# Kernel tuning notes

Measured on AMD Instinct MI355X. Metric: run time of the kernel, lower is better.

The kernel has to match this reference:

```python
import jax, jax.numpy as jnp
import numpy as np

B, S, H, E, V, T = 64, 256, 1024, 512, 10000, 64
D = H // 2  # per-direction LSTM hidden


def setup_inputs() -> dict:
    key = jax.random.key(0)
    ks = jax.random.split(key, 16)
    s = jnp.float32(0.02)
    emb = jax.random.normal(ks[4], (V, E), jnp.float32) * s
    emb = emb.at[0].set(0.0)  # padding_idx=0
    return {
        "encoder_outputs": jax.random.normal(ks[0], (B, S, H), jnp.float32),
        "enc_h0": jax.random.normal(ks[1], (2, B, D), jnp.float32),
        "enc_c0": jax.random.normal(ks[2], (2, B, D), jnp.float32),
        "target": jax.random.randint(ks[3], (B, T), 1, V),
        "mask": jnp.zeros((B, S), jnp.bool_),
        "sos_idx": 1,
        "emb": emb,
        "Wa": jax.random.normal(ks[5], (H, H), jnp.float32) * s,
        "Ua": jax.random.normal(ks[6], (H, H), jnp.float32) * s,
        "Va": jax.random.normal(ks[7], (H,), jnp.float32) * s,
        "out_W": jax.random.normal(ks[8], (V, H), jnp.float32) * s,
        "out_b": jnp.zeros((V,), jnp.float32),
        "Wih_f": jax.random.normal(ks[9], (4 * D, E + H), jnp.float32) * s,
        "Whh_f": jax.random.normal(ks[10], (4 * D, D), jnp.float32) * s,
        "bih_f": jnp.zeros((4 * D,), jnp.float32),
        "bhh_f": jnp.zeros((4 * D,), jnp.float32),
        "Wih_b": jax.random.normal(ks[11], (4 * D, E + H), jnp.float32) * s,
        "Whh_b": jax.random.normal(ks[12], (4 * D, D), jnp.float32) * s,
        "bih_b": jnp.zeros((4 * D,), jnp.float32),
        "bhh_b": jnp.zeros((4 * D,), jnp.float32),
    }


def _lstm_cell(x, h, c, Wih, Whh, bih, bhh):
    g = x @ Wih.T + h @ Whh.T + bih + bhh
    i, f, gg, o = jnp.split(g, 4, axis=-1)  # torch gate order i,f,g,o
    c2 = jax.nn.sigmoid(f) * c + jax.nn.sigmoid(i) * jnp.tanh(gg)
    h2 = jax.nn.sigmoid(o) * jnp.tanh(c2)
    return h2, c2


def reference(encoder_outputs, enc_h0, enc_c0, target, mask, sos_idx, emb, Wa, Ua, Va,
              out_W, out_b, Wih_f, Whh_f, bih_f, bhh_f, Wih_b, Whh_b, bih_b, bhh_b):
    # Cache Ua(keys) once (original recomputes it each step; math identical).
    Uk = jnp.einsum('bsh,kh->bsk', encoder_outputs, Ua)  # [B,S,H]
    b = encoder_outputs.shape[0]
    tokens = jnp.concatenate(
        [jnp.full((b, 1), sos_idx, target.dtype), target[:, :-1]], axis=1)  # [B,T]
    xs = tokens.T  # [T,B]

    def step(carry, tok):
        h, c = carry  # each [2,B,D]
        query = jnp.swapaxes(h, 0, 1).reshape(b, -1)  # [B,H] (fwd||bwd)
        sc = jnp.einsum('bsh,h->bs', jnp.tanh((query @ Wa.T)[:, None, :] + Uk), Va)
        sc = jnp.where(mask, -jnp.inf, sc)
        w = jax.nn.softmax(sc, axis=-1)  # [B,S]
        ctx = jnp.einsum('bs,bsh->bh', w, encoder_outputs)  # [B,H]
        x = jnp.concatenate([emb[tok], ctx], axis=-1)  # [B,E+H]
        hf, cf = _lstm_cell(x, h[0], c[0], Wih_f, Whh_f, bih_f, bhh_f)
        hb, cb = _lstm_cell(x, h[1], c[1], Wih_b, Whh_b, bih_b, bhh_b)
        out = jnp.concatenate([hf, hb], axis=-1)  # [B,H]
        logits = out @ out_W.T + out_b  # [B,V]
        return (jnp.stack([hf, hb]), jnp.stack([cf, cb])), (logits, w)

    (h, c), (logits, attns) = jax.lax.scan(step, (enc_h0, enc_c0), xs)
    decoder_outputs = jnp.swapaxes(logits, 0, 1)  # [B,T,V]
    attentions = jnp.swapaxes(attns, 0, 1)        # [B,T,S]
    return decoder_outputs, h, c, attentions
```

## Files before the change

kernel.cpp:

```cpp
#include <hip/hip_runtime.h>

#define NB 64
#define NS 256
#define NH 1024
#define NE 512
#define NV 10000
#define NT 64
#define ND 512
#define NEH 1536

typedef __attribute__((ext_vector_type(8))) short bf16x8;
typedef __attribute__((ext_vector_type(4))) float f32x4;

__device__ __forceinline__ short F2B(float f) {
  unsigned u = __float_as_uint(f);
  return (short)((u + 0x7fffu + ((u >> 16) & 1u)) >> 16);
}
__device__ __forceinline__ float B2F(short s) {
  return __uint_as_float(((unsigned)(unsigned short)s) << 16);
}
__device__ __forceinline__ float ftanh(float x) {
  float e = __expf(2.f * x);
  return 1.f - 2.f * __builtin_amdgcn_rcpf(e + 1.f);
}

#define GLD16(src, dst)                                                        \
  __builtin_amdgcn_global_load_lds(                                            \
      (const __attribute__((address_space(1))) void*)(src),                    \
      (__attribute__((address_space(3))) void*)(dst), 16, 0, 0)

__device__ __forceinline__ void mm64_f32a(
    const float* __restrict__ Af, int lda, const short* __restrict__ Wg,
    int ldw, int K, short* Ch, size_t ldc, char* smem)
{
  const int tid = threadIdx.x;
  const int lane = tid & 63, w = tid >> 6;
  const int qm = (w >> 1) << 5, qn = (w & 1) << 5;
  const int kg = lane >> 4, rl = lane & 15;
  f32x4 acc[2][2] = {};
  const int nIt = K >> 6;

  auto stage = [&](int k0, int buf) {
    char* As = smem + (buf << 14);
    char* Bs = As + 8192;
#pragma unroll
    for (int p = 0; p < 2; ++p) {
      int j = tid + (p << 8);
      int row = j >> 3;
      int c = (j & 7) ^ (row & 7);
      const float* src = Af + (size_t)row * lda + k0 + (c << 3);
      float4 v0 = ((const float4*)src)[0];
      float4 v1 = ((const float4*)src)[1];
      bf16x8 pk;
      pk[0] = F2B(v0.x); pk[1] = F2B(v0.y); pk[2] = F2B(v0.z); pk[3] = F2B(v0.w);
      pk[4] = F2B(v1.x); pk[5] = F2B(v1.y); pk[6] = F2B(v1.z); pk[7] = F2B(v1.w);
      *((bf16x8*)As + j) = pk;
    }
#pragma unroll
    for (int p = 0; p < 2; ++p) {
      int j = (w << 7) + (p << 6) + lane;
      int row = j >> 3;
      int c = (j & 7) ^ (row & 7);
      GLD16(Wg + (size_t)row * ldw + k0 + (c << 3), Bs + (w << 11) + (p << 10));
    }
  };

  stage(0, 0);
  for (int it = 0; it < nIt; ++it) {
    __syncthreads();
    if (it + 1 < nIt) stage((it + 1) << 6, (it + 1) & 1);
    const short* As = (const short*)(smem + ((it & 1) << 14));
    const short* Bs = As + 4096;
#pragma unroll
    for (int kk = 0; kk < 2; ++kk) {
      bf16x8 af[2], bfr[2];
#pragma unroll
      for (int mt = 0; mt < 2; ++mt) {
        int r2 = qm + (mt << 4) + rl;
        int c = (kk << 2) + kg;
        af[mt] = *((const bf16x8*)As + ((r2 << 3) | (c ^ (r2 & 7))));
      }
#pragma unroll
      for (int nt = 0; nt < 2; ++nt) {
        int r2 = qn + (nt << 4) + rl;
        int c = (kk << 2) + kg;
        bfr[nt] = *((const bf16x8*)Bs + ((r2 << 3) | (c ^ (r2 & 7))));
      }
#pragma unroll
      for (int mt = 0; mt < 2; ++mt)
#pragma unroll
        for (int nt = 0; nt < 2; ++nt)
          acc[mt][nt] = __builtin_amdgcn_mfma_f32_16x16x32_bf16(
              af[mt], bfr[nt], acc[mt][nt], 0, 0, 0);
    }
  }
#pragma unroll
  for (int mt = 0; mt < 2; ++mt)
#pragma unroll
    for (int nt = 0; nt < 2; ++nt) {
      int cn = qn + (nt << 4) + rl;
#pragma unroll
      for (int r = 0; r < 4; ++r) {
        int rowm = qm + (mt << 4) + (kg << 2) + r;
        Ch[(size_t)rowm * ldc + cn] = F2B(acc[mt][nt][r]);
      }
    }
}

__global__ __launch_bounds__(256) void uk_mm_f32(const float* __restrict__ enc,
                                                 const short* __restrict__ Ua_h,
                                                 short* __restrict__ Uk_h) {
  __shared__ char smem[32768];
  mm64_f32a(enc + (size_t)blockIdx.y * 64 * NH, NH,
            Ua_h + (size_t)blockIdx.x * 64 * NH, NH, NH,
            Uk_h + (size_t)blockIdx.y * 64 * NH + blockIdx.x * 64, NH, smem);
}

template <int MODE>
__global__ __launch_bounds__(256) void mm128(
    const short* __restrict__ A, const short* __restrict__ Bw, int nvmax,
    const float* __restrict__ bias, float* __restrict__ Cf,
    short* __restrict__ Ch)
{
  __shared__ char smem[32768];
  const int tid = threadIdx.x, lane = tid & 63, w = tid >> 6;
  const int m0 = blockIdx.y << 7;
  const int n0 = blockIdx.x << 7;
  const int qm = (w >> 1) << 6, qn = (w & 1) << 6;
  const int kg = lane >> 4, rl = lane & 15;
  f32x4 acc[4][4] = {};
  for (int k0 = 0; k0 < NH; k0 += 64) {
#pragma unroll
    for (int p = 0; p < 4; ++p) {
      int j = (((w << 2) + p) << 6) + lane;
      int row = j >> 3;
      int c = (j & 7) ^ (row & 7);
      GLD16(A + (size_t)(m0 + row) * NH + k0 + (c << 3),
            smem + (((w << 2) + p) << 10));
      int vr = n0 + row; if (vr > nvmax - 1) vr = nvmax - 1;
      GLD16(Bw + (size_t)vr * NH + k0 + (c << 3),
            smem + 16384 + (((w << 2) + p) << 10));
    }
    __syncthreads();
    const short* As = (const short*)smem;
    const short* Bs = (const short*)(smem + 16384);
#pragma unroll
    for (int kk = 0; kk < 2; ++kk) {
      bf16x8 af[4], bfr[4];
#pragma unroll
      for (int mt = 0; mt < 4; ++mt) {
        int r2 = qm + (mt << 4) + rl;
        int c = (kk << 2) + kg;
        af[mt] = *((const bf16x8*)As + ((r2 << 3) | (c ^ (r2 & 7))));
      }
#pragma unroll
      for (int nt = 0; nt < 4; ++nt) {
        int r2 = qn + (nt << 4) + rl;
        int c = (kk << 2) + kg;
        bfr[nt] = *((const bf16x8*)Bs + ((r2 << 3) | (c ^ (r2 & 7))));
      }
#pragma unroll
      for (int mt = 0; mt < 4; ++mt)
#pragma unroll
        for (int nt = 0; nt < 4; ++nt)
          acc[mt][nt] = __builtin_amdgcn_mfma_f32_16x16x32_bf16(
              af[mt], bfr[nt], acc[mt][nt], 0, 0, 0);
    }
    __syncthreads();
  }
#pragma unroll
  for (int nt = 0; nt < 4; ++nt) {
    int colv = n0 + qn + (nt << 4) + rl;
    if (colv < nvmax) {
#pragma unroll
      for (int mt = 0; mt < 4; ++mt)
#pragma unroll
        for (int r = 0; r < 4; ++r) {
          int m = m0 + qm + (mt << 4) + (kg << 2) + r;
          if (MODE == 0) {
            int b = m & 63, t = m >> 6;
            Cf[(size_t)((b << 6) + t) * NV + colv] = acc[mt][nt][r] + bias[colv];
          } else {
            Ch[(size_t)m * NH + colv] = F2B(acc[mt][nt][r]);
          }
        }
    }
  }
}

__global__ __launch_bounds__(256) void gates_v2(
    const short* __restrict__ Xt, const short* __restrict__ hcur,
    const short* __restrict__ Wcomb, const float* __restrict__ bperm,
    const float* __restrict__ cq_old, float* __restrict__ hq_f,
    float* __restrict__ cq_new, short* __restrict__ hnext)
{
  __shared__ char smem[61440];
  const int tid = threadIdx.x, lane = tid & 63, w = tid >> 6;
  const int kg = lane >> 4, rl = lane & 15;
  const int dir = blockIdx.x >> 7, gi = blockIdx.x & 127;
  const int hoff = dir << 9;
  const short* Wbase = Wcomb + (((size_t)(dir << 11) + (gi << 4)) << 11);

  auto stage = [&](int it, int buf) {
    char* dst = smem + buf * 20480;
#pragma unroll
    for (int g = 0; g < 4; ++g) {
      int row = (g << 4) + (w << 2) + kg;
      int c = rl ^ (row & 15);
      int k = (it << 7) + (c << 3);
      const short* src = (k < NEH) ? (Xt + (size_t)row * NEH + k)
                                   : (hcur + (size_t)row * NH + hoff + (k - NEH));
      GLD16(src, dst + (g << 12) + (w << 10));
    }
    {
      int rowB = (w << 2) + kg;
      int cB = rl ^ rowB;
      int kB = (it << 7) + (cB << 3);
      GLD16(Wbase + (size_t)rowB * 2048 + kB, dst + 16384 + (w << 10));
    }
  };

  stage(0, 0); stage(1, 1); stage(2, 2);
  f32x4 acc = {};
  int buf = 0;
  for (int it = 0; it < 16; ++it) {
    if (it < 14)      asm volatile("s_waitcnt vmcnt(10)" ::: "memory");
    else if (it == 14) asm volatile("s_waitcnt vmcnt(5)" ::: "memory");
    else               asm volatile("s_waitcnt vmcnt(0)" ::: "memory");
    __builtin_amdgcn_s_barrier();
    __builtin_amdgcn_sched_barrier(0);
    const short* As = (const short*)(smem + buf * 20480);
    const short* Bs = (const short*)(smem + buf * 20480 + 16384);
    const int rowA = (w << 4) + rl;
#pragma unroll
    for (int kk = 0; kk < 4; ++kk) {
      int chunk = (kk << 2) | kg;
      bf16x8 af = *((const bf16x8*)As + ((rowA << 4) | (chunk ^ (rowA & 15))));
      bf16x8 bf = *((const bf16x8*)Bs + ((rl << 4) | (chunk ^ rl)));
      acc = __builtin_amdgcn_mfma_f32_16x16x32_bf16(af, bf, acc, 0, 0, 0);
    }
    __builtin_amdgcn_sched_barrier(0);
    __builtin_amdgcn_s_barrier();
    if (it + 3 < 16) stage(it + 3, buf);
    buf = (buf == 2) ? 0 : buf + 1;
  }
  float* gacc = (float*)smem;
#pragma unroll
  for (int r = 0; r < 4; ++r)
    gacc[((w << 4) + (kg << 2) + r) * 17 + rl] = acc[r];
  __syncthreads();
  {
    const int b = tid >> 2, j2 = tid & 3;
    const float* bp = bperm + (dir << 11) + (gi << 4) + (j2 << 2);
    const float* gr = gacc + b * 17 + (j2 << 2);
    float gi_ = gr[0] + bp[0];
    float gf_ = gr[1] + bp[1];
    float gg_ = gr[2] + bp[2];
    float go_ = gr[3] + bp[3];
    const int d = ((gi >> 2) << 4) + (((gi << 2) + j2) & 15);
    const int idx = (b << 10) + hoff + d;
    float c0v = cq_old[idx];
    float si = 1.f / (1.f + __expf(-gi_));
    float sf = 1.f / (1.f + __expf(-gf_));
    float so = 1.f / (1.f + __expf(-go_));
    float tg = ftanh(gg_);
    float c2 = sf * c0v + si * tg;
    float h2 = so * ftanh(c2);
    hq_f[idx] = h2;
    cq_new[idx] = c2;
    hnext[idx] = F2B(h2);
  }
}

__global__ __launch_bounds__(256) void q_mm2(const short* __restrict__ hcur,
                                             const short* __restrict__ Wa_h,
                                             float* __restrict__ q)
{
  __shared__ char smem[61440];
  const int tid = threadIdx.x, lane = tid & 63, w = tid >> 6;
  const int kg = lane >> 4, rl = lane & 15;
  const int n0 = blockIdx.x << 4;
  const short* Wbase = Wa_h + (size_t)n0 * NH;

  auto stage = [&](int it, int buf) {
    char* dst = smem + buf * 20480;
#pragma unroll
    for (int g = 0; g < 4; ++g) {
      int row = (g << 4) + (w << 2) + kg;
      int c = rl ^ (row & 15);
      int k = (it << 7) + (c << 3);
      GLD16(hcur + (size_t)row * NH + k, dst + (g << 12) + (w << 10));
    }
    {
      int rowB = (w << 2) + kg;
      int cB = rl ^ rowB;
      int kB = (it << 7) + (cB << 3);
      GLD16(Wbase + (size_t)rowB * NH + kB, dst + 16384 + (w << 10));
    }
  };

  stage(0, 0); stage(1, 1); stage(2, 2);
  f32x4 acc = {};
  int buf = 0;
  for (int it = 0; it < 8; ++it) {
    if (it < 6)       asm volatile("s_waitcnt vmcnt(10)" ::: "memory");
    else if (it == 6) asm volatile("s_waitcnt vmcnt(5)" ::: "memory");
    else              asm volatile("s_waitcnt vmcnt(0)" ::: "memory");
    __builtin_amdgcn_s_barrier();
    __builtin_amdgcn_sched_barrier(0);
    const short* As = (const short*)(smem + buf * 20480);
    const short* Bs = (const short*)(smem + buf * 20480 + 16384);
    const int rowA = (w << 4) + rl;
#pragma unroll
    for (int kk = 0; kk < 4; ++kk) {
      int chunk = (kk << 2) | kg;
      bf16x8 af = *((const bf16x8*)As + ((rowA << 4) | (chunk ^ (rowA & 15))));
      bf16x8 bf = *((const bf16x8*)Bs + ((rl << 4) | (chunk ^ rl)));
      acc = __builtin_amdgcn_mfma_f32_16x16x32_bf16(af, bf, acc, 0, 0, 0);
    }
    __builtin_amdgcn_sched_barrier(0);
    __builtin_amdgcn_s_barrier();
    if (it + 3 < 8) stage(it + 3, buf);
    buf = (buf == 2) ? 0 : buf + 1;
  }
#pragma unroll
  for (int r = 0; r < 4; ++r)
    q[(size_t)((w << 4) + (kg << 2) + r) * NH + n0 + rl] = acc[r];
}

__global__ __launch_bounds__(256) void f2b_k(const float* __restrict__ in,
                                             short* __restrict__ out, int n4) {
  int i = blockIdx.x * 256 + threadIdx.x;
  const int stride = gridDim.x * 256;
  for (; i < n4; i += stride) {
    float4 v = ((const float4*)in)[i];
    short4 o;
    o.x = F2B(v.x); o.y = F2B(v.y); o.z = F2B(v.z); o.w = F2B(v.w);
    ((short4*)out)[i] = o;
  }
}

__global__ __launch_bounds__(256) void perm_w(
    const float* __restrict__ Wih_f, const float* __restrict__ Whh_f,
    const float* __restrict__ Wih_b, const float* __restrict__ Whh_b,
    const float* __restrict__ bih_f, const float* __restrict__ bhh_f,
    const float* __restrict__ bih_b, const float* __restrict__ bhh_b,
    short* __restrict__ Wcomb, float* __restrict__ bias_perm)
{
  int i = blockIdx.x * 256 + threadIdx.x;
  int k4 = i & 511;
  int np = (i >> 9) & 2047;
  int dir = i >> 20;
  int gate = np & 3, dlo = (np >> 2) & 15, dblk = np >> 6;
  int d = (dblk << 4) + dlo;
  int r = (gate << 9) + d;
  int k = k4 << 2;
  const float* Wih = dir ? Wih_b : Wih_f;
  const float* Whh = dir ? Whh_b : Whh_f;
  float4 v = (k < NEH) ? *(const float4*)(Wih + (size_t)r * NEH + k)
                       : *(const float4*)(Whh + (size_t)r * ND + (k - NEH));
  short4 o;
  o.x = F2B(v.x); o.y = F2B(v.y); o.z = F2B(v.z); o.w = F2B(v.w);
  *(short4*)(Wcomb + ((size_t)((dir << 11) + np) << 11) + k) = o;
  if (k4 == 0) {
    const float* bi = dir ? bih_b : bih_f;
    const float* bh = dir ? bhh_b : bhh_f;
    bias_perm[(dir << 11) + np] = bi[r] + bh[r];
  }
}

__global__ __launch_bounds__(256) void emb_fill(
    const float* __restrict__ emb, const int* __restrict__ target,
    const int* __restrict__ sos, short* __restrict__ Xbuf)
{
  int idx = blockIdx.x * 256 + threadIdx.x;
  int t = idx >> 13;
  int r = idx & 8191;
  int b = r >> 7, e4 = r & 127;
  int tok = (t == 0) ? sos[0] : target[b * NT + t - 1];
  float4 v = *(const float4*)(emb + (size_t)tok * NE + (e4 << 2));
  short4 o;
  o.x = F2B(v.x); o.y = F2B(v.y); o.z = F2B(v.z); o.w = F2B(v.w);
  *(short4*)(Xbuf + (size_t)(t * NB + b) * NEH + (e4 << 2)) = o;
}

__global__ __launch_bounds__(256) void init_state(
    const float* __restrict__ h0, const float* __restrict__ c0,
    float* __restrict__ hq, float* __restrict__ cq, short* __restrict__ H0) {
  int idx = blockIdx.x * 256 + threadIdx.x;
  int b = idx >> 10, dir = (idx >> 9) & 1, d = idx & 511;
  int src = dir * NB * ND + (b << 9) + d;
  float h = h0[src];
  hq[idx] = h;
  cq[idx] = c0[src];
  H0[idx] = F2B(h);
}

__global__ __launch_bounds__(256) void final_state(
    const float* __restrict__ hq, const float* __restrict__ cq,
    float* __restrict__ out_h, float* __restrict__ out_c) {
  int idx = blockIdx.x * 256 + threadIdx.x;
  int dir = idx >> 15, r = idx & 32767, b = r >> 9, d = r & 511;
  int src = b * NH + dir * ND + d;
  out_h[idx] = hq[src];
  out_c[idx] = cq[src];
}

__global__ __launch_bounds__(256) void attn_score(
    const float* __restrict__ q, const short* __restrict__ Uk,
    const float* __restrict__ Va, const unsigned char* __restrict__ mask,
    float* __restrict__ sc) {
  __shared__ float qs[NH];
  const int b = blockIdx.x >> 6;
  {
    int t4 = threadIdx.x << 2;
    *(float4*)(qs + t4) = *(const float4*)(q + (size_t)b * NH + t4);
  }
  __syncthreads();
  const int lane = threadIdx.x & 63, wid = threadIdx.x >> 6;
  const int bs = (blockIdx.x << 2) + wid;
  const short* ukp = Uk + (size_t)bs * NH;
  float acc = 0.f;
#pragma unroll
  for (int i = 0; i < 2; ++i) {
    int h = (i << 9) + (lane << 3);
    bf16x8 uv = *(const bf16x8*)(ukp + h);
    float4 q0 = *(const float4*)(qs + h);
    float4 q1 = *(const float4*)(qs + h + 4);
    float4 v0 = *(const float4*)(Va + h);
    float4 v1 = *(const float4*)(Va + h + 4);
    acc += v0.x * ftanh(q0.x + B2F(uv[0]));
    acc += v0.y * ftanh(q0.y + B2F(uv[1]));
    acc += v0.z * ftanh(q0.z + B2F(uv[2]));
    acc += v0.w * ftanh(q0.w + B2F(uv[3]));
    acc += v1.x * ftanh(q1.x + B2F(uv[4]));
    acc += v1.y * ftanh(q1.y + B2F(uv[5]));
    acc += v1.z * ftanh(q1.z + B2F(uv[6]));
    acc += v1.w * ftanh(q1.w + B2F(uv[7]));
  }
#pragma unroll
  for (int o = 32; o; o >>= 1) acc += __shfl_down(acc, o);
  if (lane == 0) sc[bs] = mask[bs] ? -__builtin_inff() : acc;
}

__global__ __launch_bounds__(256) void ctx_soft(
    const float* __restrict__ sc, const float* __restrict__ enc_f,
    const short* __restrict__ enc_h, int use_h,
    short* __restrict__ Xt, float* __restrict__ attn_out, int t) {
  const int tid = threadIdx.x;
  const int b = blockIdx.x >> 2, qh = blockIdx.x & 3;
  __shared__ float red[4];
  __shared__ float ws[NS];
  __shared__ float4 red4[4][64];
  float v = sc[b * NS + tid];
  float m = v;
#pragma unroll
  for (int o = 32; o; o >>= 1) m = fmaxf(m, __shfl_down(m, o));
  if ((tid & 63) == 0) red[tid >> 6] = m;
  __syncthreads();
  m = fmaxf(fmaxf(red[0], red[1]), fmaxf(red[2], red[3]));
  float e = __expf(v - m);
  float su = e;
#pragma unroll
  for (int o = 32; o; o >>= 1) su += __shfl_down(su, o);
  __syncthreads();
  if ((tid & 63) == 0) red[tid >> 6] = su;
  __syncthreads();
  su = red[0] + red[1] + red[2] + red[3];
  float wgt = e / su;
  ws[tid] = wgt;
  if (qh == 0) attn_out[((size_t)b * NT + t) * NS + tid] = wgt;
  __syncthreads();
  const int w = tid >> 6, l = tid & 63;
  const int h = (qh << 8) + (l << 2);
  const int s0 = w << 6;
  float4 a = make_float4(0.f, 0.f, 0.f, 0.f);
  if (use_h) {
    const short* ep = enc_h + ((size_t)b * NS + s0) * NH + h;
    for (int s = 0; s < 64; ++s) {
      short4 vv = *(const short4*)(ep + (size_t)s * NH);
      float wv = ws[s0 + s];
      a.x += wv * B2F(vv.x); a.y += wv * B2F(vv.y);
      a.z += wv * B2F(vv.z); a.w += wv * B2F(vv.w);
    }
  } else {
    const float* ep = enc_f + ((size_t)b * NS + s0) * NH + h;
    for (int s = 0; s < 64; ++s) {
      float4 vv = *(const float4*)(ep + (size_t)s * NH);
      float wv = ws[s0 + s];
      a.x += wv * vv.x; a.y += wv * vv.y; a.z += wv * vv.z; a.w += wv * vv.w;
    }
  }
  red4[w][l] = a;
  __syncthreads();
  if (tid < 64) {
    float4 r0 = red4[0][tid], r1 = red4[1][tid], r2 = red4[2][tid],
           r3 = red4[3][tid];
    short4 o;
    o.x = F2B(r0.x + r1.x + r2.x + r3.x);
    o.y = F2B(r0.y + r1.y + r2.y + r3.y);
    o.z = F2B(r0.z + r1.z + r2.z + r3.z);
    o.w = F2B(r0.w + r1.w + r2.w + r3.w);
    *(short4*)(Xt + (size_t)b * NEH + NE + (qh << 8) + (tid << 2)) = o;
  }
}

extern "C" void kernel_launch(void* const* d_in, const int* in_sizes, int n_in,
                              void* d_out, int out_size, void* d_ws, size_t ws_size,
                              hipStream_t stream)
{
  const float* enc    = (const float*)d_in[0];
  const float* h0     = (const float*)d_in[1];
  const float* c0     = (const float*)d_in[2];
  const int*   target = (const int*)d_in[3];
  const unsigned char* mask = (const unsigned char*)d_in[4];
  const int*   sos    = (const int*)d_in[5];
  const float* emb    = (const float*)d_in[6];
  const float* Wa     = (const float*)d_in[7];
  const float* Ua     = (const float*)d_in[8];
  const float* Va     = (const float*)d_in[9];
  const float* out_W  = (const float*)d_in[10];
  const float* out_b  = (const float*)d_in[11];
  const float* Wih_f  = (const float*)d_in[12];
  const float* Whh_f  = (const float*)d_in[13];
  const float* bih_f  = (const float*)d_in[14];
  const float* bhh_f  = (const float*)d_in[15];
  const float* Wih_b  = (const float*)d_in[16];
  const float* Whh_b  = (const float*)d_in[17];
  const float* bih_b  = (const float*)d_in[18];
  const float* bhh_b  = (const float*)d_in[19];

  float* out_dec  = (float*)d_out;
  float* out_h    = out_dec + (size_t)NB * NT * NV;
  float* out_c    = out_h + 2 * NB * ND;
  float* out_attn = out_c + 2 * NB * ND;

  char* base = (char*)d_ws;
  size_t off = 0;
  auto alloc = [&](size_t bytes) -> char* {
    char* p = base + off;
    off += (bytes + 255) & ~(size_t)255;
    return p;
  };
  short* Uk_h  = (short*)alloc((size_t)NB * NS * NH * 2);
  short* ow_h  = (short*)alloc((size_t)NV * NH * 2);
  short* Ua_h  = (short*)alloc((size_t)NH * NH * 2);
  short* Wa_h  = (short*)alloc((size_t)NH * NH * 2);
  short* Wcomb = (short*)alloc((size_t)2 * 2048 * 2048 * 2);
  float* bperm = (float*)alloc((size_t)2 * 2048 * 4);
  float* q     = (float*)alloc((size_t)NB * NH * 4);
  float* sc    = (float*)alloc((size_t)NB * NS * 4);
  short* Xbuf  = (short*)alloc((size_t)NT * NB * NEH * 2);
  float* hq    = (float*)alloc((size_t)NB * NH * 4);
  float* cq    = (float*)alloc((size_t)2 * NB * NH * 4);
  short* Hbuf  = (short*)alloc((size_t)(NT + 1) * NB * NH * 2);
  short* enc_h = nullptr;
  int use_h = 0;
  if (off + (size_t)NB * NS * NH * 2 <= ws_size) {
    enc_h = (short*)alloc((size_t)NB * NS * NH * 2);
    use_h = 1;
  }
  if (off > ws_size) return;

  f2b_k<<<dim3(2048), dim3(256), 0, stream>>>(out_W, ow_h, NV * NH / 4);
  f2b_k<<<dim3(1024), dim3(256), 0, stream>>>(Ua, Ua_h, NH * NH / 4);
  f2b_k<<<dim3(1024), dim3(256), 0, stream>>>(Wa, Wa_h, NH * NH / 4);
  perm_w<<<dim3(8192), dim3(256), 0, stream>>>(Wih_f, Whh_f, Wih_b, Whh_b,
                                               bih_f, bhh_f, bih_b, bhh_b,
                                               Wcomb, bperm);
  emb_fill<<<dim3(2048), dim3(256), 0, stream>>>(emb, target, sos, Xbuf);
  init_state<<<dim3(256), dim3(256), 0, stream>>>(h0, c0, hq, cq, Hbuf);
  if (use_h) {
    f2b_k<<<dim3(2048), dim3(256), 0, stream>>>(enc, enc_h, NB * NS * NH / 4);
    mm128<1><<<dim3(8, 128), dim3(256), 0, stream>>>(enc_h, Ua_h, NH, nullptr,
                                                     nullptr, Uk_h);
  } else {
    uk_mm_f32<<<dim3(16, 256), dim3(256), 0, stream>>>(enc, Ua_h, Uk_h);
  }

  for (int t = 0; t < NT; ++t) {
    const short* hcur = Hbuf + (size_t)t * NB * NH;
    short* hnext = Hbuf + (size_t)(t + 1) * NB * NH;
    float* cq_cur = cq + (t & 1) * (NB * NH);
    float* cq_nxt = cq + ((t & 1) ^ 1) * (NB * NH);
    short* Xt = Xbuf + (size_t)t * NB * NEH;

    q_mm2<<<dim3(64), dim3(256), 0, stream>>>(hcur, Wa_h, q);
    attn_score<<<dim3(4096), dim3(256), 0, stream>>>(q, Uk_h, Va, mask, sc);
    ctx_soft<<<dim3(256), dim3(256), 0, stream>>>(sc, enc, enc_h, use_h,
                                                  Xt, out_attn, t);
    gates_v2<<<dim3(256), dim3(256), 0, stream>>>(Xt, hcur, Wcomb, bperm,
                                                  cq_cur, hq, cq_nxt, hnext);
  }

  mm128<0><<<dim3(79, 32), dim3(256), 0, stream>>>(Hbuf + NB * NH, ow_h, NV,
                                                   out_b, out_dec, nullptr);
  final_state<<<dim3(256), dim3(256), 0, stream>>>(hq, cq, out_h, out_c);
}
```

Baseline: 2.095 ms.

## Fuse attention score, softmax and context into one per-batch kernel

Replaces the separate score kernel and softmax/context kernel with a single kernel using one 1024-thread block per batch row. Scores stay in shared memory, removing one launch per step and the global score round-trip. The grid shrinks to 64 blocks, so each block must stream its full Uk and encoder slices. This risks underusing the GPU's compute units and memory bandwidth.

```diff
diff --git a/kernel.cpp b/kernel.cpp
--- a/kernel.cpp
+++ b/kernel.cpp
@@ -328,6 +328,82 @@
     q[(size_t)((w << 4) + (kg << 2) + r) * NH + n0 + rl] = acc[r];
 }
 
+__global__ __launch_bounds__(1024) void attn_fused(
+    const float* __restrict__ q, const short* __restrict__ Uk,
+    const float* __restrict__ Va, const unsigned char* __restrict__ mask,
+    const short* __restrict__ enc_h, const float* __restrict__ enc_f,
+    int use_h, short* __restrict__ Xt, float* __restrict__ attn_out, int t)
+{
+  __shared__ float scs[NS];
+  __shared__ float ws[NS];
+  const int tid = threadIdx.x;
+  const int lane = tid & 63, w = tid >> 6;
+  const int b = blockIdx.x;
+
+  float qv[16], vv[16];
+  {
+    const float* qp = q + (size_t)b * NH + (lane << 4);
+    const float* vp = Va + (lane << 4);
+#pragma unroll
+    for (int j4 = 0; j4 < 4; ++j4) {
+      float4 a = *(const float4*)(qp + (j4 << 2));
+      float4 c = *(const float4*)(vp + (j4 << 2));
+      qv[(j4 << 2) + 0] = a.x; qv[(j4 << 2) + 1] = a.y;
+      qv[(j4 << 2) + 2] = a.z; qv[(j4 << 2) + 3] = a.w;
+      vv[(j4 << 2) + 0] = c.x; vv[(j4 << 2) + 1] = c.y;
+      vv[(j4 << 2) + 2] = c.z; vv[(j4 << 2) + 3] = c.w;
+    }
+  }
+
+#pragma unroll 1
+  for (int i = 0; i < 16; ++i) {
+    const int s = (w << 4) + i;
+    const short* up = Uk + ((size_t)b * NS + s) * NH + (lane << 4);
+    bf16x8 u0 = ((const bf16x8*)up)[0];
+    bf16x8 u1 = ((const bf16x8*)up)[1];
+    float a = 0.f;
+#pragma unroll
+    for (int j = 0; j < 8; ++j) a += vv[j] * ftanh(qv[j] + B2F(u0[j]));
+#pragma unroll
+    for (int j = 0; j < 8; ++j) a += vv[8 + j] * ftanh(qv[8 + j] + B2F(u1[j]));
+#pragma unroll
+    for (int o = 32; o; o >>= 1) a += __shfl_down(a, o);
+    if (lane == 0) scs[s] = mask[b * NS + s] ? -__builtin_inff() : a;
+  }
+  __syncthreads();
+
+  if (w == 0) {
+    float v0 = scs[lane], v1 = scs[lane + 64], v2 = scs[lane + 128],
+          v3 = scs[lane + 192];
+    float m = fmaxf(fmaxf(v0, v1), fmaxf(v2, v3));
+#pragma unroll
+    for (int o = 32; o; o >>= 1) m = fmaxf(m, __shfl_xor(m, o));
+    float e0 = __expf(v0 - m), e1 = __expf(v1 - m);
+    float e2 = __expf(v2 - m), e3 = __expf(v3 - m);
+    float su = e0 + e1 + e2 + e3;
+#pragma unroll
+    for (int o = 32; o; o >>= 1) su += __shfl_xor(su, o);
+    float inv = 1.f / su;
+    e0 *= inv; e1 *= inv; e2 *= inv; e3 *= inv;
+    ws[lane] = e0; ws[lane + 64] = e1; ws[lane + 128] = e2; ws[lane + 192] = e3;
+    float* ap = attn_out + ((size_t)b * NT + t) * NS;
+    ap[lane] = e0; ap[lane + 64] = e1; ap[lane + 128] = e2; ap[lane + 192] = e3;
+  }
+  __syncthreads();
+
+  float acc = 0.f;
+  if (use_h) {
+    const short* ep = enc_h + (size_t)b * NS * NH + tid;
+#pragma unroll 4
+    for (int s = 0; s < NS; ++s) acc += ws[s] * B2F(ep[(size_t)s * NH]);
+  } else {
+    const float* ep = enc_f + (size_t)b * NS * NH + tid;
+#pragma unroll 4
+    for (int s = 0; s < NS; ++s) acc += ws[s] * ep[(size_t)s * NH];
+  }
+  Xt[(size_t)b * NEH + NE + tid] = F2B(acc);
+}
+
 __global__ __launch_bounds__(256) void f2b_k(const float* __restrict__ in,
                                              short* __restrict__ out, int n4) {
   int i = blockIdx.x * 256 + threadIdx.x;
@@ -404,105 +480,6 @@
   int src = b * NH + dir * ND + d;
   out_h[idx] = hq[src];
   out_c[idx] = cq[src];
-}
-
-__global__ __launch_bounds__(256) void attn_score(
-    const float* __restrict__ q, const short* __restrict__ Uk,
-    const float* __restrict__ Va, const unsigned char* __restrict__ mask,
-    float* __restrict__ sc) {
-  __shared__ float qs[NH];
-  const int b = blockIdx.x >> 6;
-  {
-    int t4 = threadIdx.x << 2;
-    *(float4*)(qs + t4) = *(const float4*)(q + (size_t)b * NH + t4);
-  }
-  __syncthreads();
-  const int lane = threadIdx.x & 63, wid = threadIdx.x >> 6;
-  const int bs = (blockIdx.x << 2) + wid;
-  const short* ukp = Uk + (size_t)bs * NH;
-  float acc = 0.f;
-#pragma unroll
-  for (int i = 0; i < 2; ++i) {
-    int h = (i << 9) + (lane << 3);
-    bf16x8 uv = *(const bf16x8*)(ukp + h);
-    float4 q0 = *(const float4*)(qs + h);
-    float4 q1 = *(const float4*)(qs + h + 4);
-    float4 v0 = *(const float4*)(Va + h);
-    float4 v1 = *(const float4*)(Va + h + 4);
-    acc += v0.x * ftanh(q0.x + B2F(uv[0]));
-    acc += v0.y * ftanh(q0.y + B2F(uv[1]));
-    acc += v0.z * ftanh(q0.z + B2F(uv[2]));
-    acc += v0.w * ftanh(q0.w + B2F(uv[3]));
-    acc += v1.x * ftanh(q1.x + B2F(uv[4]));
-    acc += v1.y * ftanh(q1.y + B2F(uv[5]));
-    acc += v1.z * ftanh(q1.z + B2F(uv[6]));
-    acc += v1.w * ftanh(q1.w + B2F(uv[7]));
-  }
-#pragma unroll
-  for (int o = 32; o; o >>= 1) acc += __shfl_down(acc, o);
-  if (lane == 0) sc[bs] = mask[bs] ? -__builtin_inff() : acc;
-}
-
-__global__ __launch_bounds__(256) void ctx_soft(
-    const float* __restrict__ sc, const float* __restrict__ enc_f,
-    const short* __restrict__ enc_h, int use_h,
-    short* __restrict__ Xt, float* __restrict__ attn_out, int t) {
-  const int tid = threadIdx.x;
-  const int b = blockIdx.x >> 2, qh = blockIdx.x & 3;
-  __shared__ float red[4];
-  __shared__ float ws[NS];
-  __shared__ float4 red4[4][64];
-  float v = sc[b * NS + tid];
-  float m = v;
-#pragma unroll
-  for (int o = 32; o; o >>= 1) m = fmaxf(m, __shfl_down(m, o));
-  if ((tid & 63) == 0) red[tid >> 6] = m;
-  __syncthreads();
-  m = fmaxf(fmaxf(red[0], red[1]), fmaxf(red[2], red[3]));
-  float e = __expf(v - m);
-  float su = e;
-#pragma unroll
-  for (int o = 32; o; o >>= 1) su += __shfl_down(su, o);
-  __syncthreads();
-  if ((tid & 63) == 0) red[tid >> 6] = su;
-  __syncthreads();
-  su = red[0] + red[1] + red[2] + red[3];
-  float wgt = e / su;
-  ws[tid] = wgt;
-  if (qh == 0) attn_out[((size_t)b * NT + t) * NS + tid] = wgt;
-  __syncthreads();
-  const int w = tid >> 6, l = tid & 63;
-  const int h = (qh << 8) + (l << 2);
-  const int s0 = w << 6;
-  float4 a = make_float4(0.f, 0.f, 0.f, 0.f);
-  if (use_h) {
-    const short* ep = enc_h + ((size_t)b * NS + s0) * NH + h;
-    for (int s = 0; s < 64; ++s) {
-      short4 vv = *(const short4*)(ep + (size_t)s * NH);
-      float wv = ws[s0 + s];
-      a.x += wv * B2F(vv.x); a.y += wv * B2F(vv.y);
-      a.z += wv * B2F(vv.z); a.w += wv * B2F(vv.w);
-    }
-  } else {
-    const float* ep = enc_f + ((size_t)b * NS + s0) * NH + h;
-    for (int s = 0; s < 64; ++s) {
-      float4 vv = *(const float4*)(ep + (size_t)s * NH);
-      float wv = ws[s0 + s];
-      a.x += wv * vv.x; a.y += wv * vv.y; a.z += wv * vv.z; a.w += wv * vv.w;
-    }
-  }
-  red4[w][l] = a;
-  __syncthreads();
-  if (tid < 64) {
-    float4 r0 = red4[0][tid], r1 = red4[1][tid], r2 = red4[2][tid],
-           r3 = red4[3][tid];
-    short4 o;
-    o.x = F2B(r0.x + r1.x + r2.x + r3.x);
-    o.y = F2B(r0.y + r1.y + r2.y + r3.y);
-    o.z = F2B(r0.z + r1.z + r2.z + r3.z);
-    o.w = F2B(r0.w + r1.w + r2.w + r3.w);
-    *(short4*)(Xt + (size_t)b * NEH + NE + (qh << 8) + (tid << 2)) = o;
-  }
 }
 
 extern "C" void kernel_launch(void* const* d_in, const int* in_sizes, int n_in,
@@ -549,7 +526,6 @@
   short* Wcomb = (short*)alloc((size_t)2 * 2048 * 2048 * 2);
   float* bperm = (float*)alloc((size_t)2 * 2048 * 4);
   float* q     = (float*)alloc((size_t)NB * NH * 4);
-  float* sc    = (float*)alloc((size_t)NB * NS * 4);
   short* Xbuf  = (short*)alloc((size_t)NT * NB * NEH * 2);
   float* hq    = (float*)alloc((size_t)NB * NH * 4);
   float* cq    = (float*)alloc((size_t)2 * NB * NH * 4);
@@ -586,9 +562,9 @@
     short* Xt = Xbuf + (size_t)t * NB * NEH;
 
     q_mm2<<<dim3(64), dim3(256), 0, stream>>>(hcur, Wa_h, q);
-    attn_score<<<dim3(4096), dim3(256), 0, stream>>>(q, Uk_h, Va, mask, sc);
-    ctx_soft<<<dim3(256), dim3(256), 0, stream>>>(sc, enc, enc_h, use_h,
-                                                  Xt, out_attn, t);
+    attn_fused<<<dim3(64), dim3(1024), 0, stream>>>(q, Uk_h, Va, mask,
+                                                    enc_h, enc, use_h,
+                                                    Xt, out_attn, t);
     gates_v2<<<dim3(256), dim3(256), 0, stream>>>(Xt, hcur, Wcomb, bperm,
                                                   cq_cur, hq, cq_nxt, hnext);
   }
```

Result: slower. 4.186 ms (+99.8%).
